# Kernel optimization log

Hardware: AMD Instinct MI355X
Metric: run time of the kernel (lower is better)

## Reference

```python
import jax, jax.numpy as jnp
import numpy as np

B, N, M, KG = 2, 16384, 4096, 32
RADIUS = 0.8
CI, CL = 64, 64


def _cdist(a, b):
    # a: (B,M,3), b: (B,N,3) -> (B,M,N)
    d2 = (jnp.sum(a * a, -1)[:, :, None] + jnp.sum(b * b, -1)[:, None, :]
          - 2.0 * jnp.einsum('bmc,bnc->bmn', a, b))
    return jnp.sqrt(jnp.maximum(d2, 0.0))


def _fps(xyz, m):
    # naive sequential FPS, start index 0 (deterministic); mirrors torch loop
    b, n, _ = xyz.shape
    def step(carry, _):
        dist, far = carry
        c = jnp.take_along_axis(xyz, far[:, None, None], axis=1)  # (b,1,3)
        d = jnp.sum((xyz - c) ** 2, -1)
        dist = jnp.minimum(dist, d)
        return (dist, jnp.argmax(dist, axis=1).astype(jnp.int32)), far
    init = (jnp.full((b, n), 1e10, xyz.dtype), jnp.zeros((b,), jnp.int32))
    _, idxs = jax.lax.scan(step, init, None, length=m)
    return jnp.transpose(idxs)  # (b, m)


def setup_inputs() -> dict:
    key = jax.random.key(0)
    ks = jax.random.split(key, 32)
    def rn(i, shape, s=0.1):
        return jax.random.normal(ks[i], shape, jnp.float32) * s
    inp = {
        'xyz': jax.random.normal(ks[0], (B, N, 3), jnp.float32),
        'pts_cam': jax.random.uniform(ks[1], (B, N, 3), jnp.float32) * 80.0,
        'FI': jax.random.normal(ks[2], (B, CI, N), jnp.float32),
        'w1': rn(3, (32, 3)), 's1': jnp.ones((32,), jnp.float32), 'b1': jnp.zeros((32,), jnp.float32),
        'w2': rn(4, (32, 32)), 's2': jnp.ones((32,), jnp.float32), 'b2': jnp.zeros((32,), jnp.float32),
        'w3': rn(5, (64, 32)), 's3': jnp.ones((64,), jnp.float32), 'b3': jnp.zeros((64,), jnp.float32),
        'tw1': rn(6, (64, 1)), 'tb1': jnp.zeros((64,), jnp.float32),
        'tw2': rn(7, (64, 64)), 'tb2': jnp.zeros((64,), jnp.float32),
        'tw3': rn(8, (1, 64)), 'tb3': jnp.zeros((1,), jnp.float32),
        'gw_raw': rn(9, (64, 3)), 'gb_raw': jnp.zeros((64,), jnp.float32),
        'gw_img': rn(10, (64, 64)), 'gb_img': jnp.zeros((64,), jnp.float32),
        'gw_lid': rn(11, (64, 64)), 'gb_lid': jnp.zeros((64,), jnp.float32),
        'uw': rn(12, (1, 64)), 'ub': jnp.zeros((1,), jnp.float32),
        'vw': rn(13, (1, 64)), 'vb': jnp.zeros((1,), jnp.float32),
    }
    return inp


def reference(xyz, pts_cam, FI, w1, s1, b1, w2, s2, b2, w3, s3, b3,
              tw1, tb1, tw2, tb2, tw3, tb3,
              gw_raw, gb_raw, gw_img, gb_img, gw_lid, gb_lid, uw, ub, vw, vb):
    # --- Set abstraction: FPS + radius grouping + shared MLP + masked max ---
    idx = jax.lax.stop_gradient(_fps(xyz, M))                          # (B,M) int
    new_xyz = jnp.take_along_axis(xyz, idx[:, :, None], axis=1)        # (B,M,3)
    dists = jax.lax.stop_gradient(_cdist(new_xyz, xyz))                # (B,M,N), no_grad in torch
    negv, nidx = jax.lax.top_k(-dists, KG)                             # k nearest = argsort[:KG]
    nmask = (-negv) <= RADIUS                                          # (B,M,KG) bool
    grouped = jnp.take_along_axis(xyz[:, None], nidx[..., None], axis=2)  # (B,M,KG,3)
    g = grouped - new_xyz[:, :, None, :]                               # centered neighborhoods
    # SharedMLP2d stack (conv1x1 no-bias + BN(inference: affine) + ReLU)
    h = jax.nn.relu(jnp.einsum('bmkc,oc->bmko', g, w1) * s1 + b1)
    h = jax.nn.relu(jnp.einsum('bmkc,oc->bmko', h, w2) * s2 + b2)
    h = jax.nn.relu(jnp.einsum('bmkc,oc->bmko', h, w3) * s3 + b3)      # (B,M,KG,CL)
    h = jnp.where(nmask[..., None], h, -jnp.inf)
    FL = jnp.max(h, axis=2)                                            # (B,M,CL)
    # --- AdaptiveThresholdNet (density is constant 64/vol per the source) ---
    dens = 64.0 / (4.0 / 3.0 * 3.14159 * 1.0 ** 3)
    x = jnp.full((xyz.shape[0], 1), dens, xyz.dtype)
    t = jax.nn.relu(x @ tw1.T + tb1)
    t = jax.nn.relu(t @ tw2.T + tb2)
    t = jax.nn.sigmoid(t @ tw3.T + tb3)
    thr = 20.0 + 40.0 * t[:, 0]                                        # (B,)
    # --- DAM fusion at sampled points ---
    FI_s = jnp.take_along_axis(jnp.swapaxes(FI, 1, 2), idx[:, :, None], axis=1)  # (B,M,CI)
    fr = jax.nn.relu(new_xyz @ gw_raw.T + gb_raw)
    fi = jax.nn.relu(FI_s @ gw_img.T + gb_img)
    fl = jax.nn.relu(FL @ gw_lid.T + gb_lid)
    s = jnp.tanh(fr + fi + fl)                                         # (B,M,hid)
    wI = jax.nn.sigmoid(s @ uw.T + ub)                                 # (B,M,1)
    wL = jax.nn.sigmoid(s @ vw.T + vb)
    z = jnp.take_along_axis(pts_cam[..., 2], idx, axis=1)              # (B,M)
    near = z <= thr[:, None]
    near_f = jnp.concatenate([FL, FI_s * wI], axis=-1)                 # [FL || gated FI]
    far_f = jnp.concatenate([FI_s, FL * wL], axis=-1)                  # [FI || gated FL]
    fused = jnp.where(near[..., None], near_f, far_f)                  # (B,M,CL+CI)
    return jnp.swapaxes(fused, 1, 2)                                   # (B, CL+CI, M)
```

## Files before the change

### kernel.cpp

```cpp
#include <hip/hip_runtime.h>
#include <math.h>
#include <float.h>

#define BN   2
#define NPTS 16384
#define MPTS 4096
#define KGN  32
#define CIN  64
#define CLN  64

__device__ __forceinline__ float exadd(float a, float b) {
#pragma clang fp contract(off)
    float r = a + b; return r;
}
__device__ __forceinline__ float exsub(float a, float b) {
#pragma clang fp contract(off)
    float r = a - b; return r;
}
__device__ __forceinline__ float exmul(float a, float b) {
#pragma clang fp contract(off)
    float r = a * b; return r;
}

__device__ __forceinline__ float wave_sum64(float v) {
#pragma unroll
    for (int off = 1; off < 64; off <<= 1) v += __shfl_xor(v, off);
    return v;
}

__global__ __launch_bounds__(256) void prep_kernel(const float* __restrict__ xyz,
                                                   float4* __restrict__ pts4) {
    const int i = blockIdx.x * 256 + threadIdx.x;
    const float x = xyz[3 * i + 0];
    const float y = xyz[3 * i + 1];
    const float z = xyz[3 * i + 2];
    const float sb = exadd(exadd(exmul(x, x), exmul(y, y)), exmul(z, z));
    pts4[i] = make_float4(x, y, z, sb);
}

__global__ __attribute__((amdgpu_waves_per_eu(4, 4)))
__launch_bounds__(1024) void fps_kernel(const float4* __restrict__ P4,
                                        int* __restrict__ out_idx) {
    const int b = blockIdx.x;
    const int t = threadIdx.x;
    const float4* P = P4 + (size_t)b * NPTS;

    float px[16], py[16], pz[16], dist[16];
#pragma unroll
    for (int i = 0; i < 16; ++i) {
        float4 a = P[t * 16 + i];
        px[i] = a.x;
        py[i] = a.y;
        pz[i] = a.z;
        dist[i] = 1e10f;
    }
#pragma unroll
    for (int i = 0; i < 16; ++i) {
        asm volatile("" : "+v"(px[i]), "+v"(py[i]), "+v"(pz[i]));
    }

    __shared__ float smax[16];
    __shared__ int   swidx[2];

    if (t == 0) { swidx[0] = 0x7FFFFFFF; swidx[1] = 0x7FFFFFFF; }
    __syncthreads();

    int cidx = 0;

    for (int m = 0; m < MPTS; ++m) {
        if (t == 0) out_idx[b * MPTS + m] = cidx;

        const int ci = __builtin_amdgcn_readfirstlane(cidx);
        const float4 C = P[ci];
        const float cx = C.x, cy = C.y, cz = C.z;

        float lmax = -1.0f;
#pragma unroll
        for (int i = 0; i < 16; ++i) {
            float dx = exsub(px[i], cx);
            float dy = exsub(py[i], cy);
            float dz = exsub(pz[i], cz);
            float d  = exadd(exadd(exmul(dx, dx), exmul(dy, dy)), exmul(dz, dz));
            float nd = fminf(dist[i], d);
            dist[i] = nd;
            lmax = fmaxf(lmax, nd);
        }

        float wmax = lmax;
#pragma unroll
        for (int off = 1; off < 64; off <<= 1) wmax = fmaxf(wmax, __shfl_xor(wmax, off));
        if ((t & 63) == 0) smax[t >> 6] = wmax;

        __syncthreads();

        if (t == 0) swidx[(m + 1) & 1] = 0x7FFFFFFF;

        float bm = smax[t & 15];
#pragma unroll
        for (int off = 1; off < 16; off <<= 1) bm = fmaxf(bm, __shfl_xor(bm, off));

        if (lmax == bm) {
            int sel = 0;
#pragma unroll
            for (int i = 15; i >= 0; --i) {
                if (dist[i] == bm) sel = i;
            }
            atomicMin(&swidx[m & 1], t * 16 + sel);
        }

        __syncthreads();
        cidx = swidx[m & 1];
    }
}

__global__ __launch_bounds__(256) void knn_kernel(const float4* __restrict__ pts4,
                                                  const int* __restrict__ fps_idx,
                                                  float* __restrict__ newxyz,
                                                  int* __restrict__ nn_idx,
                                                  float* __restrict__ nn_key) {
    const int lane = threadIdx.x & 63;
    const int g    = blockIdx.x * 4 + (threadIdx.x >> 6);
    const int b    = g >> 12;
    const float4* P = pts4 + (size_t)b * NPTS;

    const int far = fps_idx[g];
    const float4 C = P[far];
    if (lane == 0) {
        newxyz[g * 3 + 0] = C.x;
        newxyz[g * 3 + 1] = C.y;
        newxyz[g * 3 + 2] = C.z;
    }
    const float sa = C.w;

    float skey = FLT_MAX;
    int   sidx = 0;

    for (int it = 0; it < NPTS / 64; ++it) {
        const int j = it * 64 + lane;
        const float4 Q = P[j];
        const float dot = exadd(exadd(exmul(C.x, Q.x), exmul(C.y, Q.y)), exmul(C.z, Q.z));
        const float d2  = exsub(exadd(sa, Q.w), exadd(dot, dot));
        const float dk  = fmaxf(d2, 0.0f);
        const float tk = __shfl(skey, 31);
        const int   ti = __shfl(sidx, 31);
        const bool pass = (sqrtf(dk) <= 0.8f) &&
                          ((dk < tk) || (dk == tk && j < ti));
        unsigned long long mask = __ballot(pass);
        while (mask) {
            const int src = __ffsll(mask) - 1;
            mask &= mask - 1;
            const float ck = __shfl(dk, src);
            const int   cj = it * 64 + src;
            const bool less = (skey < ck) || (skey == ck && sidx < cj);
            const int p = __popcll(__ballot(less));
            if (p < 32) {
                const float upk = __shfl_up(skey, 1);
                const int   upi = __shfl_up(sidx, 1);
                if (lane < 32) {
                    if (lane == p)     { skey = ck;  sidx = cj; }
                    else if (lane > p) { skey = upk; sidx = upi; }
                }
            }
        }
    }
    if (lane < KGN) {
        nn_idx[(size_t)g * KGN + lane] = sidx;
        nn_key[(size_t)g * KGN + lane] = skey;
    }
}

__global__ __attribute__((amdgpu_waves_per_eu(4, 4)))
__launch_bounds__(256) void mlp_kernel(const float* __restrict__ xyz,
                                       const float* __restrict__ w1, const float* __restrict__ s1, const float* __restrict__ b1,
                                       const float* __restrict__ w2, const float* __restrict__ s2, const float* __restrict__ b2,
                                       const float* __restrict__ w3, const float* __restrict__ s3, const float* __restrict__ b3,
                                       const float* __restrict__ newxyz,
                                       const int* __restrict__ nn_idx,
                                       const float* __restrict__ nn_key,
                                       float* __restrict__ FLout) {
    __shared__ float W1[96], S1[32], B1[32];
    __shared__ float W2[1024], S2[32], B2[32];
    __shared__ float W3[2048], S3[64], B3[64];
    const int tid = threadIdx.x;
    for (int i = tid; i < 96; i += 256)   W1[i] = w1[i];
    for (int i = tid; i < 32; i += 256) { S1[i] = s1[i]; B1[i] = b1[i]; S2[i] = s2[i]; B2[i] = b2[i]; }
    for (int i = tid; i < 1024; i += 256) W2[i] = w2[i];
    for (int i = tid; i < 2048; i += 256) W3[i] = w3[i];
    for (int i = tid; i < 64; i += 256) { S3[i] = s3[i]; B3[i] = b3[i]; }
    __syncthreads();

    const int n  = tid & 31;
    const int g  = blockIdx.x * 8 + (tid >> 5);
    const int b  = g >> 12;
    const size_t base = (size_t)g * KGN + n;
    const int   nj = nn_idx[base];
    const float nk = nn_key[base];

    const float* X = xyz + (size_t)b * NPTS * 3;
    const float gx = X[nj * 3 + 0] - newxyz[g * 3 + 0];
    const float gy = X[nj * 3 + 1] - newxyz[g * 3 + 1];
    const float gz = X[nj * 3 + 2] - newxyz[g * 3 + 2];

    float h1[32];
#pragma unroll
    for (int o = 0; o < 32; ++o) {
        float a = gx * W1[o * 3 + 0] + gy * W1[o * 3 + 1] + gz * W1[o * 3 + 2];
        h1[o] = fmaxf(a * S1[o] + B1[o], 0.0f);
    }
    float h2[32];
#pragma unroll
    for (int o = 0; o < 32; ++o) {
        float a = 0.0f;
#pragma unroll
        for (int k = 0; k < 32; ++k) a += h1[k] * W2[o * 32 + k];
        h2[o] = fmaxf(a * S2[o] + B2[o], 0.0f);
    }
    const bool valid = (sqrtf(nk) <= 0.8f);

    for (int o = 0; o < 64; ++o) {
        float a = 0.0f;
#pragma unroll
        for (int k = 0; k < 32; ++k) a += h2[k] * W3[o * 32 + k];
        float v = fmaxf(a * S3[o] + B3[o], 0.0f);
        v = valid ? v : -INFINITY;
#pragma unroll
        for (int off = 1; off < 32; off <<= 1) v = fmaxf(v, __shfl_xor(v, off));
        if (n == (o & 31)) FLout[(size_t)g * CLN + o] = v;
    }
}

__global__ __launch_bounds__(256) void fuse_kernel(const float* __restrict__ pts_cam,
                                                   const float* __restrict__ FIn,
                                                   const float* __restrict__ tw1, const float* __restrict__ tb1,
                                                   const float* __restrict__ tw2, const float* __restrict__ tb2,
                                                   const float* __restrict__ tw3, const float* __restrict__ tb3,
                                                   const float* __restrict__ gw_raw, const float* __restrict__ gb_raw,
                                                   const float* __restrict__ gw_img, const float* __restrict__ gb_img,
                                                   const float* __restrict__ gw_lid, const float* __restrict__ gb_lid,
                                                   const float* __restrict__ uw, const float* __restrict__ ub,
                                                   const float* __restrict__ vw, const float* __restrict__ vb,
                                                   const int* __restrict__ fps_idx,
                                                   const float* __restrict__ newxyz,
                                                   const float* __restrict__ FLin,
                                                   float* __restrict__ out) {
    __shared__ float WIm[4096], WLi[4096], WT2[4096];
    const int tid = threadIdx.x;
    for (int i = tid; i < 4096; i += 256) {
        int c = i >> 6, k = i & 63;
        WIm[k * 64 + c] = gw_img[i];
        WLi[k * 64 + c] = gw_lid[i];
        WT2[k * 64 + c] = tw2[i];
    }
    __syncthreads();

    const int lane = tid & 63;
    const int g    = blockIdx.x * 4 + (tid >> 6);
    const int b    = g >> 12;
    const int m    = g & (MPTS - 1);
    const int far  = fps_idx[g];

    const float fi_in = FIn[((size_t)(b * CIN + lane)) * NPTS + far];
    const float fl_in = FLin[(size_t)g * CLN + lane];
    const float nx = newxyz[g * 3 + 0], ny = newxyz[g * 3 + 1], nz = newxyz[g * 3 + 2];

    float fr = fmaxf(nx * gw_raw[lane * 3 + 0] + ny * gw_raw[lane * 3 + 1] +
                     nz * gw_raw[lane * 3 + 2] + gb_raw[lane], 0.0f);

    float ai = gb_img[lane], al = gb_lid[lane];
#pragma unroll 8
    for (int k = 0; k < 64; ++k) {
        float vi = __shfl(fi_in, k);
        float vl = __shfl(fl_in, k);
        ai += vi * WIm[k * 64 + lane];
        al += vl * WLi[k * 64 + lane];
    }
    const float s = tanhf(fr + fmaxf(ai, 0.0f) + fmaxf(al, 0.0f));

    const float dens = (float)(64.0 / (4.0 / 3.0 * 3.14159 * 1.0));
    float t1 = fmaxf(dens * tw1[lane] + tb1[lane], 0.0f);
    float a2 = tb2[lane];
#pragma unroll 8
    for (int k = 0; k < 64; ++k) a2 += __shfl(t1, k) * WT2[k * 64 + lane];
    float t2 = fmaxf(a2, 0.0f);
    float a3 = wave_sum64(t2 * tw3[lane]) + tb3[0];
    float thr = 20.0f + 40.0f * (1.0f / (1.0f + expf(-a3)));

    float aI = wave_sum64(s * uw[lane]) + ub[0];
    float aL = wave_sum64(s * vw[lane]) + vb[0];
    float wIv = 1.0f / (1.0f + expf(-aI));
    float wLv = 1.0f / (1.0f + expf(-aL));

    const float z = pts_cam[((size_t)b * NPTS + far) * 3 + 2];
    const bool near = (z <= thr);

    const size_t o1 = ((size_t)(b * 128 + lane)) * MPTS + m;
    out[o1]                       = near ? fl_in        : fi_in;
    out[o1 + (size_t)64 * MPTS]   = near ? fi_in * wIv  : fl_in * wLv;
}

extern "C" void kernel_launch(void* const* d_in, const int* in_sizes, int n_in,
                              void* d_out, int out_size, void* d_ws, size_t ws_size,
                              hipStream_t stream) {
    const float* xyz     = (const float*)d_in[0];
    const float* pts_cam = (const float*)d_in[1];
    const float* FI      = (const float*)d_in[2];
    const float* w1 = (const float*)d_in[3];
    const float* s1 = (const float*)d_in[4];
    const float* b1 = (const float*)d_in[5];
    const float* w2 = (const float*)d_in[6];
    const float* s2 = (const float*)d_in[7];
    const float* b2 = (const float*)d_in[8];
    const float* w3 = (const float*)d_in[9];
    const float* s3 = (const float*)d_in[10];
    const float* b3 = (const float*)d_in[11];
    const float* tw1 = (const float*)d_in[12];
    const float* tb1 = (const float*)d_in[13];
    const float* tw2 = (const float*)d_in[14];
    const float* tb2 = (const float*)d_in[15];
    const float* tw3 = (const float*)d_in[16];
    const float* tb3 = (const float*)d_in[17];
    const float* gw_raw = (const float*)d_in[18];
    const float* gb_raw = (const float*)d_in[19];
    const float* gw_img = (const float*)d_in[20];
    const float* gb_img = (const float*)d_in[21];
    const float* gw_lid = (const float*)d_in[22];
    const float* gb_lid = (const float*)d_in[23];
    const float* uw = (const float*)d_in[24];
    const float* ub = (const float*)d_in[25];
    const float* vw = (const float*)d_in[26];
    const float* vb = (const float*)d_in[27];
    float* out = (float*)d_out;

    char* ws = (char*)d_ws;
    int*    ws_idx    = (int*)   (ws + 0);
    float*  ws_newxyz = (float*) (ws + 32768);
    float4* ws_pts4   = (float4*)(ws + 131072);
    float*  ws_FL     = (float*) (ws + 131072);
    int*    ws_nnidx  = (int*)   (ws + 2228224);
    float*  ws_nnkey  = (float*) (ws + 3276800);
    (void)ws_size; (void)in_sizes; (void)n_in; (void)out_size;

    prep_kernel<<<(BN * NPTS) / 256, 256, 0, stream>>>(xyz, ws_pts4);
    fps_kernel<<<BN, 1024, 0, stream>>>(ws_pts4, ws_idx);
    knn_kernel<<<2048, 256, 0, stream>>>(ws_pts4, ws_idx, ws_newxyz, ws_nnidx, ws_nnkey);
    mlp_kernel<<<1024, 256, 0, stream>>>(xyz, w1, s1, b1, w2, s2, b2, w3, s3, b3,
                                         ws_newxyz, ws_nnidx, ws_nnkey, ws_FL);
    fuse_kernel<<<2048, 256, 0, stream>>>(pts_cam, FI, tw1, tb1, tw2, tb2, tw3, tb3,
                                          gw_raw, gb_raw, gw_img, gb_img, gw_lid, gb_lid,
                                          uw, ub, vw, vb, ws_idx, ws_newxyz, ws_FL, out);
}
```

Before: 7.105 ms.

## Pack FPS distance math and reduce argmax with one barrier per step

Rewrites the FPS inner loop to use packed two-wide f32 add and multiply instructions over pairs of points, halving the VALU instruction count for the distance update. It also replaces the two-barrier argmax (shared max, then atomicMin on the index) with a single-barrier scheme. Each wave ballots its first lane holding the max and writes a packed 64-bit key of (max bits, inverted index) to a double-buffered shared array. Every wave then reduces the 16 keys with 64-bit shuffles. The packed ops stay non-contracted so distances should remain bit-exact, but the 64-bit shuffle reduction adds some latency.

```diff
diff --git a/kernel.cpp b/kernel.cpp
--- a/kernel.cpp
+++ b/kernel.cpp
@@ -26,6 +26,19 @@
 #pragma unroll
     for (int off = 1; off < 64; off <<= 1) v += __shfl_xor(v, off);
     return v;
+}
+
+typedef float f32x2 __attribute__((ext_vector_type(2)));
+
+__device__ __forceinline__ f32x2 pk_add(f32x2 a, f32x2 b) {
+    f32x2 d;
+    asm("v_pk_add_f32 %0, %1, %2" : "=v"(d) : "v"(a), "v"(b));
+    return d;
+}
+__device__ __forceinline__ f32x2 pk_mul(f32x2 a, f32x2 b) {
+    f32x2 d;
+    asm("v_pk_mul_f32 %0, %1, %2" : "=v"(d) : "v"(a), "v"(b));
+    return d;
 }
 
 __global__ __launch_bounds__(256) void prep_kernel(const float* __restrict__ xyz,
@@ -43,73 +56,80 @@
                                         int* __restrict__ out_idx) {
     const int b = blockIdx.x;
     const int t = threadIdx.x;
+    const int lane = t & 63;
     const float4* P = P4 + (size_t)b * NPTS;
 
-    float px[16], py[16], pz[16], dist[16];
-#pragma unroll
-    for (int i = 0; i < 16; ++i) {
-        float4 a = P[t * 16 + i];
-        px[i] = a.x;
-        py[i] = a.y;
-        pz[i] = a.z;
-        dist[i] = 1e10f;
-    }
-#pragma unroll
-    for (int i = 0; i < 16; ++i) {
-        asm volatile("" : "+v"(px[i]), "+v"(py[i]), "+v"(pz[i]));
-    }
-
-    __shared__ float smax[16];
-    __shared__ int   swidx[2];
-
-    if (t == 0) { swidx[0] = 0x7FFFFFFF; swidx[1] = 0x7FFFFFFF; }
-    __syncthreads();
+    f32x2 px2[8], py2[8], pz2[8], dist2[8];
+#pragma unroll
+    for (int p = 0; p < 8; ++p) {
+        float4 a0 = P[t * 16 + 2 * p + 0];
+        float4 a1 = P[t * 16 + 2 * p + 1];
+        px2[p] = (f32x2){a0.x, a1.x};
+        py2[p] = (f32x2){a0.y, a1.y};
+        pz2[p] = (f32x2){a0.z, a1.z};
+        dist2[p] = (f32x2){1e10f, 1e10f};
+    }
+#pragma unroll
+    for (int p = 0; p < 8; ++p) {
+        asm volatile("" : "+v"(px2[p]), "+v"(py2[p]), "+v"(pz2[p]));
+    }
+
+    __shared__ unsigned long long swave[2][16];
 
     int cidx = 0;
 
     for (int m = 0; m < MPTS; ++m) {
-        if (t == 0) out_idx[b * MPTS + m] = cidx;
-
         const int ci = __builtin_amdgcn_readfirstlane(cidx);
         const float4 C = P[ci];
-        const float cx = C.x, cy = C.y, cz = C.z;
+        if (t == 0) out_idx[b * MPTS + m] = cidx;
+
+        const f32x2 ncx = {-C.x, -C.x};
+        const f32x2 ncy = {-C.y, -C.y};
+        const f32x2 ncz = {-C.z, -C.z};
 
         float lmax = -1.0f;
 #pragma unroll
-        for (int i = 0; i < 16; ++i) {
-            float dx = exsub(px[i], cx);
-            float dy = exsub(py[i], cy);
-            float dz = exsub(pz[i], cz);
-            float d  = exadd(exadd(exmul(dx, dx), exmul(dy, dy)), exmul(dz, dz));
-            float nd = fminf(dist[i], d);
-            dist[i] = nd;
-            lmax = fmaxf(lmax, nd);
+        for (int p = 0; p < 8; ++p) {
+            f32x2 dx = pk_add(px2[p], ncx);
+            f32x2 dy = pk_add(py2[p], ncy);
+            f32x2 dz = pk_add(pz2[p], ncz);
+            f32x2 d  = pk_add(pk_add(pk_mul(dx, dx), pk_mul(dy, dy)), pk_mul(dz, dz));
+            float n0 = fminf(dist2[p].x, d.x);
+            float n1 = fminf(dist2[p].y, d.y);
+            dist2[p].x = n0;
+            dist2[p].y = n1;
+            lmax = fmaxf(lmax, fmaxf(n0, n1));
+        }
+
+        int sel = 0;
+#pragma unroll
+        for (int p = 7; p >= 0; --p) {
+            if (dist2[p].y == lmax) sel = 2 * p + 1;
+            if (dist2[p].x == lmax) sel = 2 * p;
         }
 
         float wmax = lmax;
 #pragma unroll
         for (int off = 1; off < 64; off <<= 1) wmax = fmaxf(wmax, __shfl_xor(wmax, off));
-        if ((t & 63) == 0) smax[t >> 6] = wmax;
+
+        const unsigned long long cand = __ballot(lmax == wmax);
+        const int firstlane = __ffsll(cand) - 1;
+        if (lane == firstlane) {
+            const unsigned gidx = (unsigned)(t * 16 + sel);
+            swave[m & 1][t >> 6] =
+                ((unsigned long long)__float_as_uint(wmax) << 32) |
+                (unsigned long long)(0xFFFFFFFFu - gidx);
+        }
 
         __syncthreads();
 
-        if (t == 0) swidx[(m + 1) & 1] = 0x7FFFFFFF;
-
-        float bm = smax[t & 15];
-#pragma unroll
-        for (int off = 1; off < 16; off <<= 1) bm = fmaxf(bm, __shfl_xor(bm, off));
-
-        if (lmax == bm) {
-            int sel = 0;
-#pragma unroll
-            for (int i = 15; i >= 0; --i) {
-                if (dist[i] == bm) sel = i;
-            }
-            atomicMin(&swidx[m & 1], t * 16 + sel);
-        }
-
-        __syncthreads();
-        cidx = swidx[m & 1];
+        unsigned long long pk = swave[m & 1][t & 15];
+#pragma unroll
+        for (int off = 1; off < 16; off <<= 1) {
+            unsigned long long o = __shfl_xor(pk, off);
+            pk = (o > pk) ? o : pk;
+        }
+        cidx = (int)(0xFFFFFFFFu - (unsigned)(pk & 0xFFFFFFFFull));
     }
 }
 
```

Measured after the change: 8.914 ms. +25.5%, slower.

## Cut FPS to one barrier per iteration with packed 64-bit atomicMax argmax

Applied to the files above, without the earlier changes.

The FPS loop now packs the distance bits and inverted index into a 64-bit key. Each wave's first max lane does an atomicMax on a shared slot and writes that candidate's coordinates to shared memory. A triple-buffered slot lets each iteration use a single __syncthreads instead of two. The next centroid's coordinates come from LDS rather than a global reload. This relies on non-negative float bit ordering, and on each wave tracking only its first-lane candidate, which must match the reference's lowest-index tie-break.

```diff
diff --git a/kernel.cpp b/kernel.cpp
--- a/kernel.cpp
+++ b/kernel.cpp
@@ -43,6 +43,8 @@
                                         int* __restrict__ out_idx) {
     const int b = blockIdx.x;
     const int t = threadIdx.x;
+    const int lane = t & 63;
+    const int wid  = t >> 6;
     const float4* P = P4 + (size_t)b * NPTS;
 
     float px[16], py[16], pz[16], dist[16];
@@ -59,20 +61,22 @@
         asm volatile("" : "+v"(px[i]), "+v"(py[i]), "+v"(pz[i]));
     }
 
-    __shared__ float smax[16];
-    __shared__ int   swidx[2];
-
-    if (t == 0) { swidx[0] = 0x7FFFFFFF; swidx[1] = 0x7FFFFFFF; }
+    __shared__ unsigned long long slot[3];
+    __shared__ float4 scoord[3][16];
+
+    if (t < 3) slot[t] = 0ull;
     __syncthreads();
 
-    int cidx = 0;
+    float cx, cy, cz;
+    {
+        const float4 C0 = P[0];
+        cx = C0.x; cy = C0.y; cz = C0.z;
+    }
+    int cgidx = 0;
+    int cur = 0;
 
     for (int m = 0; m < MPTS; ++m) {
-        if (t == 0) out_idx[b * MPTS + m] = cidx;
-
-        const int ci = __builtin_amdgcn_readfirstlane(cidx);
-        const float4 C = P[ci];
-        const float cx = C.x, cy = C.y, cz = C.z;
+        if (t == 0) out_idx[b * MPTS + m] = cgidx;
 
         float lmax = -1.0f;
 #pragma unroll
@@ -89,27 +93,34 @@
         float wmax = lmax;
 #pragma unroll
         for (int off = 1; off < 64; off <<= 1) wmax = fmaxf(wmax, __shfl_xor(wmax, off));
-        if ((t & 63) == 0) smax[t >> 6] = wmax;
+
+        const unsigned long long cand = __ballot(lmax == wmax);
+        const int firstlane = __ffsll(cand) - 1;
+        if (lane == firstlane) {
+            int sel = 0;
+#pragma unroll
+            for (int i = 15; i >= 0; --i) {
+                if (dist[i] == lmax) sel = i;
+            }
+            const unsigned gidx = (unsigned)(t * 16 + sel);
+            const unsigned long long pk =
+                ((unsigned long long)__float_as_uint(wmax) << 32) |
+                (unsigned long long)(0xFFFFFFFFu - gidx);
+            atomicMax(&slot[cur], pk);
+            scoord[cur][wid] = make_float4(px[sel], py[sel], pz[sel], 0.0f);
+        }
 
         __syncthreads();
 
-        if (t == 0) swidx[(m + 1) & 1] = 0x7FFFFFFF;
-
-        float bm = smax[t & 15];
-#pragma unroll
-        for (int off = 1; off < 16; off <<= 1) bm = fmaxf(bm, __shfl_xor(bm, off));
-
-        if (lmax == bm) {
-            int sel = 0;
-#pragma unroll
-            for (int i = 15; i >= 0; --i) {
-                if (dist[i] == bm) sel = i;
-            }
-            atomicMin(&swidx[m & 1], t * 16 + sel);
-        }
-
-        __syncthreads();
-        cidx = swidx[m & 1];
+        const unsigned long long w = slot[cur];
+        if (t == 0) slot[cur == 0 ? 2 : cur - 1] = 0ull;
+
+        const unsigned gidx = 0xFFFFFFFFu - (unsigned)(w & 0xFFFFFFFFull);
+        const float4 C = scoord[cur][gidx >> 10];
+        cx = C.x; cy = C.y; cz = C.z;
+        cgidx = (int)gidx;
+
+        cur = (cur == 2) ? 0 : cur + 1;
     }
 }
 
```

New measurement: 10.49 ms. +47.6%, slower.
